# Optimization experiments

Hardware: AMD Instinct MI355X
Metric: run time of the kernel (lower is better)

The kernel has to match this reference:

```python
import math
import jax, jax.numpy as jnp
import numpy as np

# ---- config (mirrors ModelConfig) ----
B, T = 2, 2048
N_EMBD, N_HEAD, N_KV = 2048, 16, 4
DH = N_EMBD // N_HEAD          # 128
G = N_HEAD // N_KV             # 4
ROPE_THETA = 1e6
YARN_FACTOR = 64.0
ORIG_MAX_POS = 4096
BETA_FAST, BETA_SLOW = 4.0, 1.0
MSCALE, MSCALE_ALL_DIM = 1.0, 0.0


def _yarn_get_mscale(scale, mscale=1.0):
    if scale <= 1.0:
        return 1.0
    return 0.1 * mscale * math.log(scale) + 1.0


def yarn_inv_freq_and_factor():
    dim = DH
    base = ROPE_THETA
    factor = YARN_FACTOR
    if MSCALE and MSCALE_ALL_DIM:
        attn_factor = _yarn_get_mscale(factor, MSCALE) / _yarn_get_mscale(factor, MSCALE_ALL_DIM)
    else:
        attn_factor = _yarn_get_mscale(factor)

    def corr_dim(num_rot):
        return dim * math.log(ORIG_MAX_POS / (num_rot * 2 * math.pi)) / (2 * math.log(base))

    low = max(math.floor(corr_dim(BETA_FAST)), 0.0)
    high = min(math.ceil(corr_dim(BETA_SLOW)), float(dim - 1))
    if low == high:
        high += 0.001
    half = dim // 2
    t = np.arange(half, dtype=np.float32)
    ramp = np.clip((t - low) / (high - low), 0.0, 1.0)  # linear ramp
    pos = np.arange(0, dim, 2, dtype=np.float32) / dim
    pos_freqs = base ** pos
    inv_extrap = 1.0 / pos_freqs
    inv_interp = 1.0 / (factor * pos_freqs)
    extrap_factor = 1.0 - ramp
    inv = inv_interp * (1.0 - extrap_factor) + inv_extrap * extrap_factor
    return jnp.asarray(inv, jnp.float32), float(attn_factor)


INV_FREQ, ATTN_FACTOR = yarn_inv_freq_and_factor()


def apply_rope_yarn(x, positions, inv_freq, attn_factor):
    # x: [B, T, H, Dh] interleaved RoPE, then scale by attn_factor
    x32 = x.astype(jnp.float32)
    angles = positions.astype(jnp.float32)[:, None] * inv_freq[None, :]  # [T, Dh/2]
    cos = angles[None, :, None, :]  # broadcast shapes
    cos, sin = jnp.cos(cos), jnp.sin(angles)[None, :, None, :]
    x_even = x32[..., 0::2]
    x_odd = x32[..., 1::2]
    out_even = x_even * cos - x_odd * sin
    out_odd = x_even * sin + x_odd * cos
    out = jnp.stack([out_even, out_odd], axis=-1).reshape(x.shape)
    return (out * attn_factor).astype(x.dtype)


def setup_inputs() -> dict:
    key = jax.random.key(0)
    k1, k2, k3 = jax.random.split(key, 3)
    x = jax.random.normal(k1, (B, T, N_EMBD), jnp.float32)
    w_qkv = jax.random.normal(k2, (N_EMBD, N_EMBD + 2 * N_KV * DH), jnp.float32) * (N_EMBD ** -0.5)
    w_o = jax.random.normal(k3, (N_EMBD, N_EMBD), jnp.float32) * (N_EMBD ** -0.5)
    return {"x": x, "w_qkv": w_qkv, "w_o": w_o}


def reference(x, w_qkv, w_o):
    qkv = x @ w_qkv  # [B, T, n_embd + 2*n_kv*dh]
    q_raw = qkv[:, :, :N_EMBD]
    k_raw = qkv[:, :, N_EMBD:N_EMBD + N_KV * DH]
    v_raw = qkv[:, :, N_EMBD + N_KV * DH:]
    q = q_raw.reshape(B, T, N_HEAD, DH)
    k = k_raw.reshape(B, T, N_KV, DH)
    v = v_raw.reshape(B, T, N_KV, DH)

    pos = jnp.arange(T, dtype=jnp.int32)
    q = apply_rope_yarn(q, pos, INV_FREQ, ATTN_FACTOR)
    k = apply_rope_yarn(k, pos, INV_FREQ, ATTN_FACTOR)

    q = q.reshape(B, T, N_KV, G, DH).transpose(0, 2, 3, 1, 4)  # [B, kv, g, T, Dh]
    k = k.transpose(0, 2, 1, 3)  # [B, kv, T, Dh]
    v = v.transpose(0, 2, 1, 3)  # [B, kv, T, Dh]

    scale = 1.0 / math.sqrt(DH)
    att = jnp.einsum('bkgtd,bksd->bkgts', q, k) * scale
    causal = jnp.tril(jnp.ones((T, T), bool))[None, None, None]
    att = jnp.where(causal, att, jnp.asarray(-1e9, att.dtype))
    w = jax.nn.softmax(att, axis=-1)
    y = jnp.einsum('bkgts,bksd->bkgtd', w, v)
    y = y.transpose(0, 3, 1, 2, 4).reshape(B, T, N_EMBD)
    return y @ w_o
```

## Files before the change

### kernel.cpp

```cpp
#include <hip/hip_runtime.h>
#include <hip/hip_bf16.h>
#include <math.h>

#define B_    2
#define T_    2048
#define CEMB  2048
#define NH    16
#define NKV   4
#define DHD   128
#define QKVD  3072

typedef unsigned short u16;
typedef unsigned int   u32;
typedef __attribute__((ext_vector_type(8))) short  short8;
typedef __attribute__((ext_vector_type(4))) float  floatx4;

static __device__ __forceinline__ u16 f2bf(float f){
    union{float f;u32 u;}x; x.f = f; u32 u = x.u;
    return (u16)((u + 0x7fffu + ((u >> 16) & 1u)) >> 16);
}
static __device__ __forceinline__ float lo2f(u32 w){ union{u32 u;float f;}x; x.u = w << 16; return x.f; }
static __device__ __forceinline__ float hi2f(u32 w){ union{u32 u;float f;}x; x.u = w & 0xffff0000u; return x.f; }

static __device__ __forceinline__ u32 cvt_pk_bf16(float lo, float hi){
    u32 r;
    asm("v_cvt_pk_bf16_f32 %0, %1, %2" : "=v"(r) : "v"(lo), "v"(hi));
    return r;
}

static __device__ __forceinline__ void async_cp16(const u16* g, u16* lds_wave_base) {
    __builtin_amdgcn_global_load_lds(
        (const __attribute__((address_space(1))) void*)g,
        (__attribute__((address_space(3))) void*)lds_wave_base, 16, 0, 0);
}

__global__ __launch_bounds__(256) void convert_kernel(const float* __restrict__ in,
                                                      u16* __restrict__ out, int n8)
{
    const int i = blockIdx.x * 256 + threadIdx.x;
    if (i >= n8) return;
    const float4* p = reinterpret_cast<const float4*>(in);
    float4 a = p[i * 2], b = p[i * 2 + 1];
    uint4 o;
    o.x = (u32)f2bf(a.x) | ((u32)f2bf(a.y) << 16);
    o.y = (u32)f2bf(a.z) | ((u32)f2bf(a.w) << 16);
    o.z = (u32)f2bf(b.x) | ((u32)f2bf(b.y) << 16);
    o.w = (u32)f2bf(b.z) | ((u32)f2bf(b.w) << 16);
    reinterpret_cast<uint4*>(out)[i] = o;
}

__global__ __launch_bounds__(256) void transpose_f32_bf16(const float* __restrict__ in,
                                                          u16* __restrict__ out,
                                                          int R, int Cn)
{
    __shared__ float tl[32][33];
    const int tx = threadIdx.x & 31, ty = threadIdx.x >> 5;
    const int c0 = blockIdx.x << 5, r0 = blockIdx.y << 5;
    #pragma unroll
    for (int i = 0; i < 4; ++i)
        tl[ty + i * 8][tx] = in[(size_t)(r0 + ty + i * 8) * Cn + c0 + tx];
    __syncthreads();
    #pragma unroll
    for (int i = 0; i < 4; ++i)
        out[(size_t)(c0 + ty + i * 8) * R + r0 + tx] = f2bf(tl[tx][ty + i * 8]);
}

__global__ __launch_bounds__(256) void vt_build_kernel(const u16* __restrict__ qkv,
                                                       u16* __restrict__ vt)
{
    __shared__ u16 tl[32][33];
    const int tx = threadIdx.x & 31, ty = threadIdx.x >> 5;
    const int t0 = blockIdx.x << 5, d0 = blockIdx.y << 5;
    const int b = blockIdx.z >> 2, kv = blockIdx.z & 3;
    #pragma unroll
    for (int i = 0; i < 4; ++i)
        tl[ty + i * 8][tx] =
            qkv[(size_t)(b * T_ + t0 + ty + i * 8) * QKVD + CEMB + NKV * DHD + kv * DHD + d0 + tx];
    __syncthreads();
    #pragma unroll
    for (int i = 0; i < 4; ++i)
        vt[(size_t)((b * NKV + kv) * DHD + d0 + ty + i * 8) * T_ + t0 + tx] = tl[tx][ty + i * 8];
}

template <bool F32OUT>
__global__ __launch_bounds__(256) void gemm_mfma_kernel(const u16* __restrict__ A,
                                                        const u16* __restrict__ BT,
                                                        void* __restrict__ Cv,
                                                        int M, int N, int K)
{
    __shared__ u16 As[128 * 32];
    __shared__ u16 Bs[128 * 32];
    const int tid  = threadIdx.x;
    const int lane = tid & 63;
    const int wv   = tid >> 6;
    const int n16  = lane & 15;
    const int quad = lane >> 4;
    const int wm   = wv >> 1, wn = wv & 1;
    const int row0 = blockIdx.y << 7;
    const int col0 = blockIdx.x << 7;

    floatx4 acc[4][4];
    #pragma unroll
    for (int i = 0; i < 4; ++i)
        #pragma unroll
        for (int j = 0; j < 4; ++j) acc[i][j] = (floatx4)0.0f;

    for (int k0 = 0; k0 < K; k0 += 32) {
        __syncthreads();
        #pragma unroll
        for (int it = 0; it < 2; ++it) {
            const int idx = it * 256 + tid;
            const int m = idx >> 2, k8 = (idx & 3) << 3;
            async_cp16(A  + (size_t)(row0 + m) * K + k0 + k8, &As[(it * 256 + wv * 64) * 8]);
            async_cp16(BT + (size_t)(col0 + m) * K + k0 + k8, &Bs[(it * 256 + wv * 64) * 8]);
        }
        __syncthreads();
        short8 af[4], bf[4];
        #pragma unroll
        for (int mt = 0; mt < 4; ++mt)
            af[mt] = *reinterpret_cast<const short8*>(&As[(wm * 64 + mt * 16 + n16) * 32 + quad * 8]);
        #pragma unroll
        for (int nt = 0; nt < 4; ++nt)
            bf[nt] = *reinterpret_cast<const short8*>(&Bs[(wn * 64 + nt * 16 + n16) * 32 + quad * 8]);
        #pragma unroll
        for (int mt = 0; mt < 4; ++mt)
            #pragma unroll
            for (int nt = 0; nt < 4; ++nt)
                acc[mt][nt] = __builtin_amdgcn_mfma_f32_16x16x32_bf16(af[mt], bf[nt], acc[mt][nt], 0, 0, 0);
    }
    #pragma unroll
    for (int mt = 0; mt < 4; ++mt) {
        #pragma unroll
        for (int r = 0; r < 4; ++r) {
            const int row = row0 + wm * 64 + mt * 16 + quad * 4 + r;
            if (F32OUT) {
                float* C = reinterpret_cast<float*>(Cv);
                #pragma unroll
                for (int nt = 0; nt < 4; ++nt)
                    C[(size_t)row * N + col0 + wn * 64 + nt * 16 + n16] = acc[mt][nt][r];
            } else {
                u16* C = reinterpret_cast<u16*>(Cv);
                #pragma unroll
                for (int nt = 0; nt < 4; ++nt)
                    C[(size_t)row * N + col0 + wn * 64 + nt * 16 + n16] = f2bf(acc[mt][nt][r]);
            }
        }
    }
}

__global__ __launch_bounds__(256) void rope_kernel(
    u16* __restrict__ qkv, const float attn_factor, const float low, const float high)
{
    const int total = B_ * T_ * (NH + NKV) * (DHD / 2);
    int idx = blockIdx.x * 256 + threadIdx.x;
    if (idx >= total) return;
    const int d = idx & 63;
    int r = idx >> 6;
    const int h = r % (NH + NKV);
    r /= (NH + NKV);
    const int t = r % T_;
    const int b = r / T_;
    const int off = (h < NH) ? (h * DHD) : (CEMB + (h - NH) * DHD);

    u32* p = reinterpret_cast<u32*>(qkv + (size_t)(b * T_ + t) * QKVD + off) + d;
    u32 w = *p;
    float xe = lo2f(w), xo = hi2f(w);

    float df   = (float)d;
    float ramp = (df - low) / (high - low);
    ramp = fminf(fmaxf(ramp, 0.0f), 1.0f);
    float pf     = expf((2.0f * df / 128.0f) * 13.815510557964274f);
    float inv_ex = 1.0f / pf;
    float inv    = inv_ex * ((1.0f / 64.0f) * ramp + (1.0f - ramp));
    float ang = (float)t * inv;
    float s = sinf(ang), c = cosf(ang);
    float oe = (xe * c - xo * s) * attn_factor;
    float oo = (xe * s + xo * c) * attn_factor;
    *p = (u32)f2bf(oe) | ((u32)f2bf(oo) << 16);
}

__global__ __launch_bounds__(256, 2) void attn_mfma_kernel(const u16* __restrict__ qkv,
                                                           const u16* __restrict__ vt,
                                                           u16* __restrict__ y)
{
    __shared__ __align__(16) u16 Ksd[2][64 * 128];
    __shared__ __align__(16) u16 Vtsd[2][128 * 64];
    __shared__ u16 Pl[4 * 16 * 72];

    const int tid  = threadIdx.x;
    const int lane = tid & 63;
    const int wv   = tid >> 6;
    const int n16  = lane & 15;
    const int quad = lane >> 4;
    const int nx   = blockIdx.x;
    const int bh   = blockIdx.y;
    const int b    = bh >> 4;
    const int h    = bh & 15;
    const int kh   = h >> 2;

    const float C1 = 0.08838834764831845f * 1.4426950408889634f;

    u16* plw = Pl + wv * 16 * 72;
    const u16* kbase = qkv + (size_t)(b * T_) * QKVD + CEMB + kh * DHD;
    const u16* vbase = vt + (size_t)((b * NKV + kh) * DHD) * T_;

    auto dma_k = [&](int j0, int buf) {
        #pragma unroll
        for (int it = 0; it < 4; ++it) {
            const int P   = it * 256 + tid;
            const int row = P >> 4;
            const int lc  = (P & 15) ^ (row & 15);
            async_cp16(kbase + (size_t)(j0 + row) * QKVD + (lc << 3),
                       &Ksd[buf][(it * 256 + wv * 64) * 8]);
        }
    };
    auto dma_v = [&](int j0, int buf) {
        #pragma unroll
        for (int it = 0; it < 4; ++it) {
            const int P   = it * 256 + tid;
            const int row = P >> 3;
            const int lc  = (P & 7) ^ (row & 7);
            async_cp16(vbase + (size_t)row * T_ + j0 + (lc << 3),
                       &Vtsd[buf][(it * 256 + wv * 64) * 8]);
        }
    };

    #pragma unroll
    for (int qt = 0; qt < 2; ++qt) {
        const int i0 = ((qt == 0) ? (31 - nx) : nx) << 6;

        const int qrow = i0 + wv * 16 + n16;
        const u16* qp = qkv + (size_t)(b * T_ + qrow) * QKVD + h * DHD;
        short8 qf[4];
        #pragma unroll
        for (int kk = 0; kk < 4; ++kk)
            qf[kk] = *reinterpret_cast<const short8*>(qp + kk * 32 + quad * 8);

        floatx4 oacc[8];
        #pragma unroll
        for (int i = 0; i < 8; ++i) oacc[i] = (floatx4)0.0f;
        float m_cur = -INFINITY, l_cur = 0.0f;

        __syncthreads();
        dma_k(0, 0);
        dma_v(0, 0);

        for (int j0 = 0; j0 <= i0; j0 += 64) {
            const int buf = (j0 >> 6) & 1;
            __syncthreads();
            if (j0 + 64 <= i0) {
                dma_k(j0 + 64, buf ^ 1);
                dma_v(j0 + 64, buf ^ 1);
            }
            const u16* kb = Ksd[buf];
            const u16* vb = Vtsd[buf];

            floatx4 st[4];
            #pragma unroll
            for (int t = 0; t < 4; ++t) st[t] = (floatx4)0.0f;
            __builtin_amdgcn_s_setprio(1);
            #pragma unroll
            for (int t = 0; t < 4; ++t) {
                #pragma unroll
                for (int kk = 0; kk < 4; ++kk) {
                    short8 a = *reinterpret_cast<const short8*>(
                        &kb[(t * 16 + n16) * 128 + (((kk * 4 + quad) ^ n16) << 3)]);
                    st[t] = __builtin_amdgcn_mfma_f32_16x16x32_bf16(a, qf[kk], st[t], 0, 0, 0);
                }
            }
            __builtin_amdgcn_s_setprio(0);

            const bool diag = (j0 + 63 > i0 + wv * 16);
            float tmax = -INFINITY;
            #pragma unroll
            for (int t = 0; t < 4; ++t) {
                if (diag) {
                    #pragma unroll
                    for (int r = 0; r < 4; ++r) {
                        const int key = j0 + t * 16 + quad * 4 + r;
                        if (key > qrow) st[t][r] = -INFINITY;
                    }
                }
                tmax = fmaxf(tmax,
                             fmaxf(fmaxf(st[t][0], st[t][1]), fmaxf(st[t][2], st[t][3])));
            }
            tmax = fmaxf(tmax, __shfl_xor(tmax, 16));
            tmax = fmaxf(tmax, __shfl_xor(tmax, 32));

            if (!__all((tmax - m_cur) * C1 <= 8.0f)) {
                const float mnew  = fmaxf(m_cur, tmax);
                const float alpha = exp2f((m_cur - mnew) * C1);
                m_cur = mnew;
                l_cur *= alpha;
                #pragma unroll
                for (int dt = 0; dt < 8; ++dt) {
                    oacc[dt][0] *= alpha; oacc[dt][1] *= alpha;
                    oacc[dt][2] *= alpha; oacc[dt][3] *= alpha;
                }
            }

            const float mC = m_cur * C1;
            float lsum = 0.0f;
            #pragma unroll
            for (int t = 0; t < 4; ++t) {
                float p0 = exp2f(fmaf(st[t][0], C1, -mC));
                float p1 = exp2f(fmaf(st[t][1], C1, -mC));
                float p2 = exp2f(fmaf(st[t][2], C1, -mC));
                float p3 = exp2f(fmaf(st[t][3], C1, -mC));
                lsum += (p0 + p1) + (p2 + p3);
                uint2 pk;
                pk.x = cvt_pk_bf16(p0, p1);
                pk.y = cvt_pk_bf16(p2, p3);
                *reinterpret_cast<uint2*>(&plw[n16 * 72 + t * 16 + quad * 4]) = pk;
            }
            lsum += __shfl_xor(lsum, 16);
            lsum += __shfl_xor(lsum, 32);
            l_cur += lsum;

            __builtin_amdgcn_s_setprio(1);
            #pragma unroll
            for (int kt = 0; kt < 2; ++kt) {
                short8 pfrag = *reinterpret_cast<const short8*>(&plw[n16 * 72 + kt * 32 + quad * 8]);
                #pragma unroll
                for (int dt = 0; dt < 8; ++dt) {
                    short8 vfrag = *reinterpret_cast<const short8*>(
                        &vb[(dt * 16 + n16) * 64 + (((kt * 4 + quad) ^ (n16 & 7)) << 3)]);
                    oacc[dt] = __builtin_amdgcn_mfma_f32_16x16x32_bf16(vfrag, pfrag, oacc[dt], 0, 0, 0);
                }
            }
            __builtin_amdgcn_s_setprio(0);
        }

        const float linv = 1.0f / l_cur;
        u16* yp = y + (size_t)(b * T_ + qrow) * CEMB + h * DHD + quad * 4;
        #pragma unroll
        for (int dt = 0; dt < 8; ++dt) {
            float a0 = oacc[dt][0] * linv, a1 = oacc[dt][1] * linv;
            float a2 = oacc[dt][2] * linv, a3 = oacc[dt][3] * linv;
            u32 w0 = cvt_pk_bf16(a0, a1);
            u32 w1 = cvt_pk_bf16(a2, a3);
            *reinterpret_cast<u32*>(yp + dt * 16)     = w0;
            *reinterpret_cast<u32*>(yp + dt * 16 + 2) = w1;
        }
    }
}

extern "C" void kernel_launch(void* const* d_in, const int* in_sizes, int n_in,
                              void* d_out, int out_size, void* d_ws, size_t ws_size,
                              hipStream_t stream) {
    const size_t NX   = (size_t)B_ * T_ * CEMB;
    const size_t NWQ  = (size_t)CEMB * QKVD;
    const size_t NWO  = (size_t)CEMB * CEMB;
    const size_t NQKV = (size_t)B_ * T_ * QKVD;
    const size_t NY   = NX;

    u16* qkv = (u16*)d_ws;
    u16* y   = qkv + NQKV;
    u16* xb  = y + NY;
    u16* wqT = xb + NX;
    u16* woT = wqT + NWQ;
    u16* vtb = xb;

    convert_kernel<<<(int)(NX / 8 + 255) / 256, 256, 0, stream>>>((const float*)d_in[0], xb, (int)(NX / 8));
    transpose_f32_bf16<<<dim3(QKVD / 32, CEMB / 32), 256, 0, stream>>>((const float*)d_in[1], wqT, CEMB, QKVD);
    transpose_f32_bf16<<<dim3(CEMB / 32, CEMB / 32), 256, 0, stream>>>((const float*)d_in[2], woT, CEMB, CEMB);

    gemm_mfma_kernel<false><<<dim3(QKVD / 128, (B_ * T_) / 128), 256, 0, stream>>>(
        xb, wqT, qkv, B_ * T_, QKVD, CEMB);

    const double two_pi = 6.283185307179586476925286766559;
    double corr4 = 128.0 * log(4096.0 / (4.0 * two_pi)) / (2.0 * log(1.0e6));
    double corr1 = 128.0 * log(4096.0 / (1.0 * two_pi)) / (2.0 * log(1.0e6));
    double lowd  = floor(corr4); if (lowd < 0.0) lowd = 0.0;
    double highd = ceil(corr1);  if (highd > 127.0) highd = 127.0;
    if (lowd == highd) highd += 0.001;
    float attn_factor = (float)(0.1 * log(64.0) + 1.0);

    const int rope_total = B_ * T_ * (NH + NKV) * (DHD / 2);
    rope_kernel<<<(rope_total + 255) / 256, 256, 0, stream>>>(
        qkv, attn_factor, (float)lowd, (float)highd);

    vt_build_kernel<<<dim3(T_ / 32, DHD / 32, B_ * NKV), 256, 0, stream>>>(qkv, vtb);

    attn_mfma_kernel<<<dim3(T_ / 128, B_ * NH), 256, 0, stream>>>(qkv, vtb, y);

    gemm_mfma_kernel<true><<<dim3(CEMB / 128, (B_ * T_) / 128), 256, 0, stream>>>(
        y, woT, d_out, B_ * T_, CEMB, CEMB);
}
```

Before: 327.8 us.

## Process both causal query tiles concurrently in 512-thread attention blocks

The attention kernel now launches 512 threads per block: waves 0-3 take the late (long) query tile and waves 4-7 the early (short) tile, sharing one K/V stream instead of processing the two tiles one after another. K/V tiles loaded for the short tile are reused by the long tile, halving global K/V traffic per pair, and the block is swizzled so that neighbouring blocks map to different heads and batches. The P scratch buffer switches from padding to an XOR swizzle. The short-tile waves idle through the later iterations while still hitting the barriers, and launch bounds of 512x4 tighten register limits.

Result: faster. 320.9 us (-2.1%).

```diff
diff --git a/kernel.cpp b/kernel.cpp
--- a/kernel.cpp
+++ b/kernel.cpp
@@ -179,169 +179,175 @@
     *p = (u32)f2bf(oe) | ((u32)f2bf(oo) << 16);
 }
 
-__global__ __launch_bounds__(256, 2) void attn_mfma_kernel(const u16* __restrict__ qkv,
+__global__ __launch_bounds__(512, 4) void attn_mfma_kernel(const u16* __restrict__ qkv,
                                                            const u16* __restrict__ vt,
                                                            u16* __restrict__ y)
 {
     __shared__ __align__(16) u16 Ksd[2][64 * 128];
     __shared__ __align__(16) u16 Vtsd[2][128 * 64];
-    __shared__ u16 Pl[4 * 16 * 72];
+    __shared__ __align__(16) u16 Pl[8 * 1024];
 
     const int tid  = threadIdx.x;
     const int lane = tid & 63;
     const int wv   = tid >> 6;
     const int n16  = lane & 15;
     const int quad = lane >> 4;
-    const int nx   = blockIdx.x;
-    const int bh   = blockIdx.y;
-    const int b    = bh >> 4;
-    const int h    = bh & 15;
-    const int kh   = h >> 2;
+
+    const int lin = blockIdx.y * 16 + blockIdx.x;
+    const int swz = (lin & 7) * 64 + (lin >> 3);
+    const int nx  = swz & 15;
+    const int bh  = swz >> 4;
+    const int b   = bh >> 4;
+    const int h   = bh & 15;
+    const int kh  = h >> 2;
 
     const float C1 = 0.08838834764831845f * 1.4426950408889634f;
 
-    u16* plw = Pl + wv * 16 * 72;
+    u16* plw = Pl + wv * 1024;
+    const int psw = (n16 & 7) << 3;
+
     const u16* kbase = qkv + (size_t)(b * T_) * QKVD + CEMB + kh * DHD;
     const u16* vbase = vt + (size_t)((b * NKV + kh) * DHD) * T_;
 
     auto dma_k = [&](int j0, int buf) {
         #pragma unroll
-        for (int it = 0; it < 4; ++it) {
-            const int P   = it * 256 + tid;
+        for (int it = 0; it < 2; ++it) {
+            const int P   = it * 512 + tid;
             const int row = P >> 4;
             const int lc  = (P & 15) ^ (row & 15);
             async_cp16(kbase + (size_t)(j0 + row) * QKVD + (lc << 3),
-                       &Ksd[buf][(it * 256 + wv * 64) * 8]);
+                       &Ksd[buf][(it * 512 + wv * 64) * 8]);
         }
     };
     auto dma_v = [&](int j0, int buf) {
         #pragma unroll
-        for (int it = 0; it < 4; ++it) {
-            const int P   = it * 256 + tid;
+        for (int it = 0; it < 2; ++it) {
+            const int P   = it * 512 + tid;
             const int row = P >> 3;
             const int lc  = (P & 7) ^ (row & 7);
             async_cp16(vbase + (size_t)row * T_ + j0 + (lc << 3),
-                       &Vtsd[buf][(it * 256 + wv * 64) * 8]);
+                       &Vtsd[buf][(it * 512 + wv * 64) * 8]);
         }
     };
 
-    #pragma unroll
-    for (int qt = 0; qt < 2; ++qt) {
-        const int i0 = ((qt == 0) ? (31 - nx) : nx) << 6;
-
-        const int qrow = i0 + wv * 16 + n16;
-        const u16* qp = qkv + (size_t)(b * T_ + qrow) * QKVD + h * DHD;
-        short8 qf[4];
-        #pragma unroll
-        for (int kk = 0; kk < 4; ++kk)
-            qf[kk] = *reinterpret_cast<const short8*>(qp + kk * 32 + quad * 8);
-
-        floatx4 oacc[8];
-        #pragma unroll
-        for (int i = 0; i < 8; ++i) oacc[i] = (floatx4)0.0f;
-        float m_cur = -INFINITY, l_cur = 0.0f;
-
+    const int i0H = (31 - nx) << 6;
+    const int i0  = (wv < 4) ? i0H : (nx << 6);
+    const int qb  = i0 + (wv & 3) * 16;
+    const int qrow = qb + n16;
+
+    const u16* qp = qkv + (size_t)(b * T_ + qrow) * QKVD + h * DHD;
+    short8 qf[4];
+    #pragma unroll
+    for (int kk = 0; kk < 4; ++kk)
+        qf[kk] = *reinterpret_cast<const short8*>(qp + kk * 32 + quad * 8);
+
+    floatx4 oacc[8];
+    #pragma unroll
+    for (int i = 0; i < 8; ++i) oacc[i] = (floatx4)0.0f;
+    float m_cur = -INFINITY, l_cur = 0.0f;
+
+    dma_k(0, 0);
+    dma_v(0, 0);
+
+    for (int j0 = 0; j0 <= i0H; j0 += 64) {
+        const int buf = (j0 >> 6) & 1;
         __syncthreads();
-        dma_k(0, 0);
-        dma_v(0, 0);
-
-        for (int j0 = 0; j0 <= i0; j0 += 64) {
-            const int buf = (j0 >> 6) & 1;
-            __syncthreads();
-            if (j0 + 64 <= i0) {
-                dma_k(j0 + 64, buf ^ 1);
-                dma_v(j0 + 64, buf ^ 1);
-            }
-            const u16* kb = Ksd[buf];
-            const u16* vb = Vtsd[buf];
-
-            floatx4 st[4];
+        if (j0 + 64 <= i0H) {
+            dma_k(j0 + 64, buf ^ 1);
+            dma_v(j0 + 64, buf ^ 1);
+        }
+        if (j0 > i0) continue;
+
+        const u16* kb = Ksd[buf];
+        const u16* vb = Vtsd[buf];
+
+        floatx4 st[4];
+        #pragma unroll
+        for (int t = 0; t < 4; ++t) st[t] = (floatx4)0.0f;
+        __builtin_amdgcn_s_setprio(1);
+        #pragma unroll
+        for (int t = 0; t < 4; ++t) {
             #pragma unroll
-            for (int t = 0; t < 4; ++t) st[t] = (floatx4)0.0f;
-            __builtin_amdgcn_s_setprio(1);
+            for (int kk = 0; kk < 4; ++kk) {
+                short8 a = *reinterpret_cast<const short8*>(
+                    &kb[(t * 16 + n16) * 128 + (((kk * 4 + quad) ^ n16) << 3)]);
+                st[t] = __builtin_amdgcn_mfma_f32_16x16x32_bf16(a, qf[kk], st[t], 0, 0, 0);
+            }
+        }
+        __builtin_amdgcn_s_setprio(0);
+
+        const bool diag = (j0 + 63 > qb);
+        float tmax = -INFINITY;
+        #pragma unroll
+        for (int t = 0; t < 4; ++t) {
+            if (diag) {
+                #pragma unroll
+                for (int r = 0; r < 4; ++r) {
+                    const int key = j0 + t * 16 + quad * 4 + r;
+                    if (key > qrow) st[t][r] = -INFINITY;
+                }
+            }
+            tmax = fmaxf(tmax,
+                         fmaxf(fmaxf(st[t][0], st[t][1]), fmaxf(st[t][2], st[t][3])));
+        }
+        tmax = fmaxf(tmax, __shfl_xor(tmax, 16));
+        tmax = fmaxf(tmax, __shfl_xor(tmax, 32));
+
+        if (!__all((tmax - m_cur) * C1 <= 8.0f)) {
+            const float mnew  = fmaxf(m_cur, tmax);
+            const float alpha = exp2f((m_cur - mnew) * C1);
+            m_cur = mnew;
+            l_cur *= alpha;
             #pragma unroll
-            for (int t = 0; t < 4; ++t) {
-                #pragma unroll
-                for (int kk = 0; kk < 4; ++kk) {
-                    short8 a = *reinterpret_cast<const short8*>(
-                        &kb[(t * 16 + n16) * 128 + (((kk * 4 + quad) ^ n16) << 3)]);
-                    st[t] = __builtin_amdgcn_mfma_f32_16x16x32_bf16(a, qf[kk], st[t], 0, 0, 0);
-                }
-            }
-            __builtin_amdgcn_s_setprio(0);
-
-            const bool diag = (j0 + 63 > i0 + wv * 16);
-            float tmax = -INFINITY;
+            for (int dt = 0; dt < 8; ++dt) {
+                oacc[dt][0] *= alpha; oacc[dt][1] *= alpha;
+                oacc[dt][2] *= alpha; oacc[dt][3] *= alpha;
+            }
+        }
+
+        const float mC = m_cur * C1;
+        float lsum = 0.0f;
+        #pragma unroll
+        for (int t = 0; t < 4; ++t) {
+            float p0 = exp2f(fmaf(st[t][0], C1, -mC));
+            float p1 = exp2f(fmaf(st[t][1], C1, -mC));
+            float p2 = exp2f(fmaf(st[t][2], C1, -mC));
+            float p3 = exp2f(fmaf(st[t][3], C1, -mC));
+            lsum += (p0 + p1) + (p2 + p3);
+            uint2 pk;
+            pk.x = cvt_pk_bf16(p0, p1);
+            pk.y = cvt_pk_bf16(p2, p3);
+            *reinterpret_cast<uint2*>(&plw[n16 * 64 + ((t * 16 + quad * 4) ^ psw)]) = pk;
+        }
+        lsum += __shfl_xor(lsum, 16);
+        lsum += __shfl_xor(lsum, 32);
+        l_cur += lsum;
+
+        __builtin_amdgcn_s_setprio(1);
+        #pragma unroll
+        for (int kt = 0; kt < 2; ++kt) {
+            short8 pfrag = *reinterpret_cast<const short8*>(
+                &plw[n16 * 64 + ((kt * 32 + quad * 8) ^ psw)]);
             #pragma unroll
-            for (int t = 0; t < 4; ++t) {
-                if (diag) {
-                    #pragma unroll
-                    for (int r = 0; r < 4; ++r) {
-                        const int key = j0 + t * 16 + quad * 4 + r;
-                        if (key > qrow) st[t][r] = -INFINITY;
-                    }
-                }
-                tmax = fmaxf(tmax,
-                             fmaxf(fmaxf(st[t][0], st[t][1]), fmaxf(st[t][2], st[t][3])));
-            }
-            tmax = fmaxf(tmax, __shfl_xor(tmax, 16));
-            tmax = fmaxf(tmax, __shfl_xor(tmax, 32));
-
-            if (!__all((tmax - m_cur) * C1 <= 8.0f)) {
-                const float mnew  = fmaxf(m_cur, tmax);
-                const float alpha = exp2f((m_cur - mnew) * C1);
-                m_cur = mnew;
-                l_cur *= alpha;
-                #pragma unroll
-                for (int dt = 0; dt < 8; ++dt) {
-                    oacc[dt][0] *= alpha; oacc[dt][1] *= alpha;
-                    oacc[dt][2] *= alpha; oacc[dt][3] *= alpha;
-                }
-            }
-
-            const float mC = m_cur * C1;
-            float lsum = 0.0f;
-            #pragma unroll
-            for (int t = 0; t < 4; ++t) {
-                float p0 = exp2f(fmaf(st[t][0], C1, -mC));
-                float p1 = exp2f(fmaf(st[t][1], C1, -mC));
-                float p2 = exp2f(fmaf(st[t][2], C1, -mC));
-                float p3 = exp2f(fmaf(st[t][3], C1, -mC));
-                lsum += (p0 + p1) + (p2 + p3);
-                uint2 pk;
-                pk.x = cvt_pk_bf16(p0, p1);
-                pk.y = cvt_pk_bf16(p2, p3);
-                *reinterpret_cast<uint2*>(&plw[n16 * 72 + t * 16 + quad * 4]) = pk;
-            }
-            lsum += __shfl_xor(lsum, 16);
-            lsum += __shfl_xor(lsum, 32);
-            l_cur += lsum;
-
-            __builtin_amdgcn_s_setprio(1);
-            #pragma unroll
-            for (int kt = 0; kt < 2; ++kt) {
-                short8 pfrag = *reinterpret_cast<const short8*>(&plw[n16 * 72 + kt * 32 + quad * 8]);
-                #pragma unroll
-                for (int dt = 0; dt < 8; ++dt) {
-                    short8 vfrag = *reinterpret_cast<const short8*>(
-                        &vb[(dt * 16 + n16) * 64 + (((kt * 4 + quad) ^ (n16 & 7)) << 3)]);
-                    oacc[dt] = __builtin_amdgcn_mfma_f32_16x16x32_bf16(vfrag, pfrag, oacc[dt], 0, 0, 0);
-                }
-            }
-            __builtin_amdgcn_s_setprio(0);
-        }
-
-        const float linv = 1.0f / l_cur;
-        u16* yp = y + (size_t)(b * T_ + qrow) * CEMB + h * DHD + quad * 4;
-        #pragma unroll
-        for (int dt = 0; dt < 8; ++dt) {
-            float a0 = oacc[dt][0] * linv, a1 = oacc[dt][1] * linv;
-            float a2 = oacc[dt][2] * linv, a3 = oacc[dt][3] * linv;
-            u32 w0 = cvt_pk_bf16(a0, a1);
-            u32 w1 = cvt_pk_bf16(a2, a3);
-            *reinterpret_cast<u32*>(yp + dt * 16)     = w0;
-            *reinterpret_cast<u32*>(yp + dt * 16 + 2) = w1;
-        }
+            for (int dt = 0; dt < 8; ++dt) {
+                short8 vfrag = *reinterpret_cast<const short8*>(
+                    &vb[(dt * 16 + n16) * 64 + (((kt * 4 + quad) ^ (n16 & 7)) << 3)]);
+                oacc[dt] = __builtin_amdgcn_mfma_f32_16x16x32_bf16(vfrag, pfrag, oacc[dt], 0, 0, 0);
+            }
+        }
+        __builtin_amdgcn_s_setprio(0);
+    }
+
+    const float linv = 1.0f / l_cur;
+    u16* yp = y + (size_t)(b * T_ + qrow) * CEMB + h * DHD + quad * 4;
+    #pragma unroll
+    for (int dt = 0; dt < 8; ++dt) {
+        float a0 = oacc[dt][0] * linv, a1 = oacc[dt][1] * linv;
+        float a2 = oacc[dt][2] * linv, a3 = oacc[dt][3] * linv;
+        u32 w0 = cvt_pk_bf16(a0, a1);
+        u32 w1 = cvt_pk_bf16(a2, a3);
+        *reinterpret_cast<u32*>(yp + dt * 16)     = w0;
+        *reinterpret_cast<u32*>(yp + dt * 16 + 2) = w1;
     }
 }
 
@@ -382,7 +388,7 @@
 
     vt_build_kernel<<<dim3(T_ / 32, DHD / 32, B_ * NKV), 256, 0, stream>>>(qkv, vtb);
 
-    attn_mfma_kernel<<<dim3(T_ / 128, B_ * NH), 256, 0, stream>>>(qkv, vtb, y);
+    attn_mfma_kernel<<<dim3(T_ / 128, B_ * NH), 512, 0, stream>>>(qkv, vtb, y);
 
     gemm_mfma_kernel<true><<<dim3(CEMB / 128, (B_ * T_) / 128), 256, 0, stream>>>(
         y, woT, d_out, B_ * T_, CEMB, CEMB);
```
